# Performance work log

Measured on AMD Instinct MI355X. Metric: run time of the kernel, lower is better.

Reference implementation:

```python
import jax, jax.numpy as jnp
import numpy as np

N_NODES = 50000
N_EDGES = 800000
IN_FEATS = 256
H_FEATS = 256
NUM_CLASSES = 16
NUM_GRAPHS = 64


def _glorot(key, shape):
    lim = float(np.sqrt(6.0 / (shape[0] + shape[1])))
    return jax.random.uniform(key, shape, jnp.float32, -lim, lim)


def setup_inputs() -> dict:
    key = jax.random.key(0)
    ks = jax.random.split(key, 12)
    x = jax.random.normal(ks[0], (N_NODES, IN_FEATS), jnp.float32)
    edge_index = jax.random.randint(ks[1], (2, N_EDGES), 0, N_NODES, jnp.int64)
    batch_vec = jnp.sort(jax.random.randint(ks[2], (N_NODES,), 0, NUM_GRAPHS, jnp.int64))
    W1 = _glorot(ks[3], (IN_FEATS, H_FEATS)); b1 = jnp.zeros((H_FEATS,), jnp.float32)
    W2 = _glorot(ks[4], (H_FEATS, H_FEATS)); b2 = jnp.zeros((H_FEATS,), jnp.float32)
    W3 = _glorot(ks[5], (H_FEATS, H_FEATS)); b3 = jnp.zeros((H_FEATS,), jnp.float32)
    W4 = _glorot(ks[6], (H_FEATS, NUM_CLASSES)); b4 = jnp.zeros((NUM_CLASSES,), jnp.float32)
    return {"x": x, "edge_index": edge_index, "batch_vec": batch_vec,
            "W1": W1, "b1": b1, "W2": W2, "b2": b2,
            "W3": W3, "b3": b3, "W4": W4, "b4": b4}


def gcn_conv(x, W, b, src, dst, deg_inv_sqrt):
    # PyG GCNConv: out = D^{-1/2} (A + I) D^{-1/2} (x W) + b
    h = x @ W  # [N, F_out]
    norm = deg_inv_sqrt[src] * deg_inv_sqrt[dst]  # [E+N]
    msgs = h[src] * norm[:, None]  # gather + scale
    agg = jax.ops.segment_sum(msgs, dst, num_segments=x.shape[0])
    return agg + b


def reference(x, edge_index, batch_vec, W1, b1, W2, b2, W3, b3, W4, b4):
    n = x.shape[0]
    # add self-loops once (shared across layers)
    loops = jnp.arange(n, dtype=edge_index.dtype)
    src = jnp.concatenate([edge_index[0], loops])
    dst = jnp.concatenate([edge_index[1], loops])
    deg = jax.ops.segment_sum(jnp.ones_like(dst, dtype=x.dtype), dst, num_segments=n)
    deg_inv_sqrt = jnp.where(deg > 0, jax.lax.rsqrt(deg), 0.0)

    h = gcn_conv(x, W1, b1, src, dst, deg_inv_sqrt)
    h_copy = jax.nn.relu(h)
    # dropout is identity in eval mode (training=False)
    h = gcn_conv(h_copy, W2, b2, src, dst, deg_inv_sqrt)
    h_copy = jax.nn.relu(jax.nn.relu(h) + h_copy)
    h = gcn_conv(h_copy, W3, b3, src, dst, deg_inv_sqrt)
    h = jax.nn.relu(jax.nn.relu(h) + h_copy)
    h = gcn_conv(h, W4, b4, src, dst, deg_inv_sqrt)

    # global_mean_pool over batch vector
    sums = jax.ops.segment_sum(h, batch_vec, num_segments=NUM_GRAPHS)
    counts = jax.ops.segment_sum(jnp.ones((n,), h.dtype), batch_vec, num_segments=NUM_GRAPHS)
    return sums / jnp.maximum(counts, 1.0)[:, None]
```

## Files before the change

kernel.cpp:

```cpp
#include <hip/hip_runtime.h>
#include <hip/hip_bf16.h>

#define N_NODES 50000
#define N_EDGES 800000
#define F 256
#define NGRAPH 64
#define NCLS 16
#define NBLK_N 196

typedef short short8 __attribute__((ext_vector_type(8)));
typedef float f32x4 __attribute__((ext_vector_type(4)));

__device__ __forceinline__ float bf2f(ushort u) {
    unsigned v = ((unsigned)u) << 16;
    return __uint_as_float(v);
}
__device__ __forceinline__ ushort f2bf(float f) {
    __hip_bfloat16 b = __float2bfloat16(f);
    return *reinterpret_cast<ushort*>(&b);
}


__global__ __launch_bounds__(256) void k_zero_int(int* __restrict__ p, int n) {
    int i = blockIdx.x * 256 + threadIdx.x;
    if (i < n) p[i] = 0;
}

__global__ __launch_bounds__(256) void k_count(const int* __restrict__ dst,
                                               int* __restrict__ ecnt) {
    int e = blockIdx.x * 256 + threadIdx.x;
    if (e < N_EDGES) atomicAdd(&ecnt[dst[e]], 1);
}

__global__ __launch_bounds__(256) void k_dinv(const int* __restrict__ ecnt,
                                              float* __restrict__ dinv) {
    int n = blockIdx.x * 256 + threadIdx.x;
    if (n < N_NODES) dinv[n] = rsqrtf((float)(ecnt[n] + 1));
}

__global__ __launch_bounds__(256) void k_scan_block(const int* __restrict__ ecnt,
                                                    int* __restrict__ rowptr,
                                                    int* __restrict__ blkSum) {
    __shared__ int sh[256];
    int i = blockIdx.x * 256 + threadIdx.x;
    int v = (i < N_NODES) ? ecnt[i] : 0;
    sh[threadIdx.x] = v;
    __syncthreads();
#pragma unroll
    for (int off = 1; off < 256; off <<= 1) {
        int t = (threadIdx.x >= off) ? sh[threadIdx.x - off] : 0;
        __syncthreads();
        sh[threadIdx.x] += t;
        __syncthreads();
    }
    if (i < N_NODES) rowptr[i] = sh[threadIdx.x] - v;
    if (threadIdx.x == 255) blkSum[blockIdx.x] = sh[255];
}

__global__ __launch_bounds__(256) void k_scan_tops(int* __restrict__ blkSum,
                                                   int* __restrict__ blkOff) {
    __shared__ int sh[256];
    int v = (threadIdx.x < NBLK_N) ? blkSum[threadIdx.x] : 0;
    sh[threadIdx.x] = v;
    __syncthreads();
#pragma unroll
    for (int off = 1; off < 256; off <<= 1) {
        int t = (threadIdx.x >= off) ? sh[threadIdx.x - off] : 0;
        __syncthreads();
        sh[threadIdx.x] += t;
        __syncthreads();
    }
    if (threadIdx.x < NBLK_N) blkOff[threadIdx.x] = sh[threadIdx.x] - v;
}

__global__ __launch_bounds__(256) void k_scan_add(int* __restrict__ rowptr,
                                                  const int* __restrict__ blkOff,
                                                  int* __restrict__ cursor) {
    int i = blockIdx.x * 256 + threadIdx.x;
    if (i < N_NODES) {
        int r = rowptr[i] + blkOff[blockIdx.x];
        rowptr[i] = r;
        cursor[i] = r;
    }
    if (i == 0) rowptr[N_NODES] = N_EDGES;
}

__global__ __launch_bounds__(256) void k_fill_csr(const int* __restrict__ src,
                                                  const int* __restrict__ dst,
                                                  const float* __restrict__ dinv,
                                                  int* __restrict__ cursor,
                                                  int* __restrict__ csr_src,
                                                  float* __restrict__ csr_w) {
    int e = blockIdx.x * 256 + threadIdx.x;
    if (e >= N_EDGES) return;
    int s = src[e];
    int d = dst[e];
    int p = atomicAdd(&cursor[d], 1);
    csr_src[p] = s;
    csr_w[p] = dinv[s] * dinv[d];
}


__global__ __launch_bounds__(256) void k_cast_bf16(const float* __restrict__ in,
                                                   ushort* __restrict__ out,
                                                   int n8) {
    int i = blockIdx.x * 256 + threadIdx.x;
    if (i >= n8) return;
    const float4* ip = (const float4*)(in + (size_t)i * 8);
    float4 a = ip[0], b = ip[1];
    short8 v;
    v[0] = (short)f2bf(a.x); v[1] = (short)f2bf(a.y);
    v[2] = (short)f2bf(a.z); v[3] = (short)f2bf(a.w);
    v[4] = (short)f2bf(b.x); v[5] = (short)f2bf(b.y);
    v[6] = (short)f2bf(b.z); v[7] = (short)f2bf(b.w);
    *(short8*)(out + (size_t)i * 8) = v;
}

__global__ __launch_bounds__(256) void k_wpack(const float* __restrict__ W,
                                               ushort* __restrict__ Wp) {
    int idx = blockIdx.x * 256 + threadIdx.x;
    if (idx >= 16 * 8 * 64) return;
    int lane = idx & 63;
    int ks = (idx >> 6) & 7;
    int ctg = idx >> 9;
    int kbase = ks * 32 + (lane >> 4) * 8;
    int col = ctg * 16 + (lane & 15);
    short8 v;
#pragma unroll
    for (int e = 0; e < 8; ++e)
        v[e] = (short)f2bf(W[(size_t)(kbase + e) * 256 + col]);
    *(short8*)(Wp + (size_t)idx * 8) = v;
}


__global__ __launch_bounds__(256, 2) void k_mfma256(const ushort* __restrict__ Ab,
                                                    const ushort* __restrict__ Wp,
                                                    ushort* __restrict__ C) {
    const int t = threadIdx.x;
    const int wv = t >> 6;
    const int l = t & 63;
    const int m0 = blockIdx.x * 64;
    const int colbase = wv * 64;
    const int lrow = l & 15;
    const int lk = (l >> 4) * 8;

    short8 wf[4][8];
    const short8* wp = (const short8*)Wp;
#pragma unroll
    for (int ct = 0; ct < 4; ++ct)
#pragma unroll
        for (int ks = 0; ks < 8; ++ks)
            wf[ct][ks] = wp[(size_t)(((wv * 4 + ct) * 8 + ks) * 64) + l];

#pragma unroll
    for (int msub = 0; msub < 4; ++msub) {
        int arow = m0 + msub * 16 + lrow;
        if (arow >= N_NODES) arow = N_NODES - 1;
        const ushort* ap = Ab + (size_t)arow * F + lk;
        short8 af[8];
#pragma unroll
        for (int ks = 0; ks < 8; ++ks)
            af[ks] = *(const short8*)(ap + ks * 32);

        f32x4 acc[4];
#pragma unroll
        for (int ct = 0; ct < 4; ++ct) acc[ct] = (f32x4){0.f, 0.f, 0.f, 0.f};
#pragma unroll
        for (int ks = 0; ks < 8; ++ks)
#pragma unroll
            for (int ct = 0; ct < 4; ++ct)
                acc[ct] = __builtin_amdgcn_mfma_f32_16x16x32_bf16(af[ks], wf[ct][ks], acc[ct], 0, 0, 0);

        int orow0 = m0 + msub * 16 + (l >> 4) * 4;
#pragma unroll
        for (int ct = 0; ct < 4; ++ct) {
            int ocol = colbase + ct * 16 + (l & 15);
#pragma unroll
            for (int r = 0; r < 4; ++r) {
                int orow = orow0 + r;
                if (orow < N_NODES)
                    C[(size_t)orow * F + ocol] = f2bf(acc[ct][r]);
            }
        }
    }
}


template <int MODE>
__global__ __launch_bounds__(256) void k_gather256(const ushort* __restrict__ H,
                                                   const float* __restrict__ bias,
                                                   const float* __restrict__ dinv,
                                                   const int* __restrict__ rowptr,
                                                   const int* __restrict__ csr_src,
                                                   const float* __restrict__ csr_w,
                                                   const ushort* __restrict__ hc,
                                                   ushort* __restrict__ OUT) {
    int gid = blockIdx.x * 256 + threadIdx.x;
    int n = gid >> 6;
    int lane = gid & 63;
    if (n >= N_NODES) return;
    int c = lane * 4;

    float di = dinv[n];
    float s = di * di;
    const ushort4 h = *(const ushort4*)(H + (size_t)n * F + c);
    const float4 b = *(const float4*)(bias + c);
    float ax = b.x + bf2f(h.x) * s;
    float ay = b.y + bf2f(h.y) * s;
    float az = b.z + bf2f(h.z) * s;
    float aw = b.w + bf2f(h.w) * s;

    int i = rowptr[n];
    const int end = rowptr[n + 1];
    for (; i + 3 < end; i += 4) {
        int s0 = csr_src[i], s1 = csr_src[i + 1], s2 = csr_src[i + 2], s3 = csr_src[i + 3];
        float w0 = csr_w[i], w1 = csr_w[i + 1], w2 = csr_w[i + 2], w3 = csr_w[i + 3];
        const ushort4 v0 = *(const ushort4*)(H + (size_t)s0 * F + c);
        const ushort4 v1 = *(const ushort4*)(H + (size_t)s1 * F + c);
        const ushort4 v2 = *(const ushort4*)(H + (size_t)s2 * F + c);
        const ushort4 v3 = *(const ushort4*)(H + (size_t)s3 * F + c);
        ax += w0 * bf2f(v0.x) + w1 * bf2f(v1.x) + w2 * bf2f(v2.x) + w3 * bf2f(v3.x);
        ay += w0 * bf2f(v0.y) + w1 * bf2f(v1.y) + w2 * bf2f(v2.y) + w3 * bf2f(v3.y);
        az += w0 * bf2f(v0.z) + w1 * bf2f(v1.z) + w2 * bf2f(v2.z) + w3 * bf2f(v3.z);
        aw += w0 * bf2f(v0.w) + w1 * bf2f(v1.w) + w2 * bf2f(v2.w) + w3 * bf2f(v3.w);
    }
    for (; i < end; ++i) {
        int s0 = csr_src[i];
        float w0 = csr_w[i];
        const ushort4 v0 = *(const ushort4*)(H + (size_t)s0 * F + c);
        ax += w0 * bf2f(v0.x); ay += w0 * bf2f(v0.y);
        az += w0 * bf2f(v0.z); aw += w0 * bf2f(v0.w);
    }

    float ox, oy, oz, ow;
    if (MODE == 1) {
        ox = fmaxf(ax, 0.f); oy = fmaxf(ay, 0.f);
        oz = fmaxf(az, 0.f); ow = fmaxf(aw, 0.f);
    } else {
        const ushort4 hv = *(const ushort4*)(hc + (size_t)n * F + c);
        ox = fmaxf(fmaxf(ax, 0.f) + bf2f(hv.x), 0.f);
        oy = fmaxf(fmaxf(ay, 0.f) + bf2f(hv.y), 0.f);
        oz = fmaxf(fmaxf(az, 0.f) + bf2f(hv.z), 0.f);
        ow = fmaxf(fmaxf(aw, 0.f) + bf2f(hv.w), 0.f);
    }
    ushort4 ov;
    ov.x = f2bf(ox); ov.y = f2bf(oy); ov.z = f2bf(oz); ov.w = f2bf(ow);
    *(ushort4*)(OUT + (size_t)n * F + c) = ov;
}


__global__ __launch_bounds__(256) void k_gemm16(const ushort* __restrict__ A,
                                                const float* __restrict__ W4,
                                                float* __restrict__ C) {
    __shared__ float Ws[256][16];
    const int t = threadIdx.x;
    {
        const float4* wp = (const float4*)(W4 + (size_t)t * 16);
        float4 a = wp[0], b = wp[1], c = wp[2], d = wp[3];
        float4* sp = (float4*)&Ws[t][0];
        sp[0] = a; sp[1] = b; sp[2] = c; sp[3] = d;
    }
    __syncthreads();
    int row = blockIdx.x * 256 + t;
    if (row >= N_NODES) return;
    const short8* ap = (const short8*)(A + (size_t)row * F);
    float acc[16];
#pragma unroll
    for (int c = 0; c < 16; ++c) acc[c] = 0.f;
    for (int k8 = 0; k8 < 32; ++k8) {
        short8 a8 = ap[k8];
#pragma unroll
        for (int j = 0; j < 8; ++j) {
            float av = bf2f((ushort)a8[j]);
            const float4* wr = (const float4*)&Ws[k8 * 8 + j][0];
            float4 w0 = wr[0], w1 = wr[1], w2 = wr[2], w3 = wr[3];
            acc[0]  += av * w0.x; acc[1]  += av * w0.y;
            acc[2]  += av * w0.z; acc[3]  += av * w0.w;
            acc[4]  += av * w1.x; acc[5]  += av * w1.y;
            acc[6]  += av * w1.z; acc[7]  += av * w1.w;
            acc[8]  += av * w2.x; acc[9]  += av * w2.y;
            acc[10] += av * w2.z; acc[11] += av * w2.w;
            acc[12] += av * w3.x; acc[13] += av * w3.y;
            acc[14] += av * w3.z; acc[15] += av * w3.w;
        }
    }
    float4* op = (float4*)(C + (size_t)row * 16);
    op[0] = make_float4(acc[0], acc[1], acc[2], acc[3]);
    op[1] = make_float4(acc[4], acc[5], acc[6], acc[7]);
    op[2] = make_float4(acc[8], acc[9], acc[10], acc[11]);
    op[3] = make_float4(acc[12], acc[13], acc[14], acc[15]);
}

__global__ __launch_bounds__(256) void k_gather16(const float* __restrict__ H16,
                                                  const float* __restrict__ bias,
                                                  const float* __restrict__ dinv,
                                                  const int* __restrict__ rowptr,
                                                  const int* __restrict__ csr_src,
                                                  const float* __restrict__ csr_w,
                                                  float* __restrict__ OUT) {
    int gid = blockIdx.x * 256 + threadIdx.x;
    int n = gid >> 2;
    int q = (gid & 3) * 4;
    if (n >= N_NODES) return;

    float di = dinv[n];
    float s = di * di;
    const float4 h = *(const float4*)(H16 + (size_t)n * 16 + q);
    const float4 b = *(const float4*)(bias + q);
    float ax = b.x + h.x * s, ay = b.y + h.y * s, az = b.z + h.z * s, aw = b.w + h.w * s;

    const int end = rowptr[n + 1];
    for (int i = rowptr[n]; i < end; ++i) {
        int s0 = csr_src[i];
        float w0 = csr_w[i];
        const float4 v = *(const float4*)(H16 + (size_t)s0 * 16 + q);
        ax += w0 * v.x; ay += w0 * v.y; az += w0 * v.z; aw += w0 * v.w;
    }
    *(float4*)(OUT + (size_t)n * 16 + q) = make_float4(ax, ay, az, aw);
}


__global__ __launch_bounds__(256) void k_pool_zero(float* __restrict__ pool,
                                                   float* __restrict__ cnt) {
    int i = blockIdx.x * 256 + threadIdx.x;
    if (i < NGRAPH * NCLS) pool[i] = 0.f;
    if (i < NGRAPH) cnt[i] = 0.f;
}

__global__ __launch_bounds__(256) void k_pool(const float* __restrict__ H4,
                                              const int* __restrict__ batch,
                                              float* __restrict__ pool,
                                              float* __restrict__ cnt) {
    __shared__ float ps[NGRAPH][NCLS];
    __shared__ float pc[NGRAPH];
    for (int i = threadIdx.x; i < NGRAPH * NCLS; i += 256) ((float*)ps)[i] = 0.f;
    if (threadIdx.x < NGRAPH) pc[threadIdx.x] = 0.f;
    __syncthreads();
    int n = blockIdx.x * 256 + threadIdx.x;
    if (n < N_NODES) {
        int g = batch[n];
        const float4* hp = (const float4*)(H4 + (size_t)n * 16);
        float4 a = hp[0], b = hp[1], c = hp[2], d = hp[3];
        atomicAdd(&ps[g][0],  a.x); atomicAdd(&ps[g][1],  a.y);
        atomicAdd(&ps[g][2],  a.z); atomicAdd(&ps[g][3],  a.w);
        atomicAdd(&ps[g][4],  b.x); atomicAdd(&ps[g][5],  b.y);
        atomicAdd(&ps[g][6],  b.z); atomicAdd(&ps[g][7],  b.w);
        atomicAdd(&ps[g][8],  c.x); atomicAdd(&ps[g][9],  c.y);
        atomicAdd(&ps[g][10], c.z); atomicAdd(&ps[g][11], c.w);
        atomicAdd(&ps[g][12], d.x); atomicAdd(&ps[g][13], d.y);
        atomicAdd(&ps[g][14], d.z); atomicAdd(&ps[g][15], d.w);
        atomicAdd(&pc[g], 1.f);
    }
    __syncthreads();
    for (int i = threadIdx.x; i < NGRAPH * NCLS; i += 256)
        unsafeAtomicAdd(&pool[i], ((float*)ps)[i]);
    if (threadIdx.x < NGRAPH) unsafeAtomicAdd(&cnt[threadIdx.x], pc[threadIdx.x]);
}

__global__ __launch_bounds__(256) void k_final(const float* __restrict__ pool,
                                               const float* __restrict__ cnt,
                                               float* __restrict__ out) {
    int i = blockIdx.x * 256 + threadIdx.x;
    if (i < NGRAPH * NCLS) out[i] = pool[i] / fmaxf(cnt[i >> 4], 1.f);
}


extern "C" void kernel_launch(void* const* d_in, const int* in_sizes, int n_in,
                              void* d_out, int out_size, void* d_ws, size_t ws_size,
                              hipStream_t stream) {
    const float* x   = (const float*)d_in[0];
    const int*   ei  = (const int*)d_in[1];
    const int*   bvec= (const int*)d_in[2];
    const float* W1  = (const float*)d_in[3];
    const float* b1  = (const float*)d_in[4];
    const float* W2  = (const float*)d_in[5];
    const float* b2  = (const float*)d_in[6];
    const float* W3  = (const float*)d_in[7];
    const float* b3  = (const float*)d_in[8];
    const float* W4  = (const float*)d_in[9];
    const float* b4  = (const float*)d_in[10];
    float* out = (float*)d_out;

    const int* src = ei;
    const int* dst = ei + N_EDGES;

    const size_t NF = (size_t)N_NODES * F;
    float* ws = (float*)d_ws;
    ushort* XA = (ushort*)ws;
    ushort* XB = XA + NF;
    ushort* Hg = XB + NF;
    float*  G16 = (float*)(Hg + NF);
    float*  H4  = G16 + (size_t)N_NODES * 16;
    float* aux  = H4 + (size_t)N_NODES * 16;
    int*   ecnt   = (int*)aux;
    float* dinv   = aux + N_NODES;
    int*   rowptr = (int*)(aux + 2 * N_NODES);
    int*   cursor = (int*)(aux + 3 * N_NODES + 64);
    int*   blkSum = (int*)(aux + 4 * N_NODES + 64);
    int*   blkOff = blkSum + 256;
    int*   csr_src= blkOff + 256;
    float* csr_w  = (float*)(csr_src + N_EDGES);
    float* pool   = csr_w + N_EDGES;
    float* cnt    = pool + NGRAPH * NCLS;
    ushort* Wp1   = (ushort*)(cnt + NGRAPH);
    ushort* Wp2   = Wp1 + 65536;
    ushort* Wp3   = Wp2 + 65536;

    const int BN = NBLK_N;
    const int BE = (N_EDGES + 255) / 256;
    const int BG = (N_NODES * 64 + 255) / 256;
    const int BM = (N_NODES + 63) / 64;
    const int BC = (int)((NF / 8 + 255) / 256);

    k_cast_bf16<<<BC, 256, 0, stream>>>(x, XA, (int)(NF / 8));
    k_wpack<<<32, 256, 0, stream>>>(W1, Wp1);
    k_wpack<<<32, 256, 0, stream>>>(W2, Wp2);
    k_wpack<<<32, 256, 0, stream>>>(W3, Wp3);

    k_zero_int<<<BN, 256, 0, stream>>>(ecnt, N_NODES);
    k_count<<<BE, 256, 0, stream>>>(dst, ecnt);
    k_dinv<<<BN, 256, 0, stream>>>(ecnt, dinv);
    k_scan_block<<<BN, 256, 0, stream>>>(ecnt, rowptr, blkSum);
    k_scan_tops<<<1, 256, 0, stream>>>(blkSum, blkOff);
    k_scan_add<<<BN, 256, 0, stream>>>(rowptr, blkOff, cursor);
    k_fill_csr<<<BE, 256, 0, stream>>>(src, dst, dinv, cursor, csr_src, csr_w);

    k_mfma256<<<BM, 256, 0, stream>>>(XA, Wp1, Hg);
    k_gather256<1><<<BG, 256, 0, stream>>>(Hg, b1, dinv, rowptr, csr_src, csr_w, nullptr, XB);

    k_mfma256<<<BM, 256, 0, stream>>>(XB, Wp2, Hg);
    k_gather256<2><<<BG, 256, 0, stream>>>(Hg, b2, dinv, rowptr, csr_src, csr_w, XB, XA);

    k_mfma256<<<BM, 256, 0, stream>>>(XA, Wp3, Hg);
    k_gather256<2><<<BG, 256, 0, stream>>>(Hg, b3, dinv, rowptr, csr_src, csr_w, XA, XB);

    k_gemm16<<<BN, 256, 0, stream>>>(XB, W4, G16);
    k_gather16<<<(N_NODES * 4 + 255) / 256, 256, 0, stream>>>(G16, b4, dinv, rowptr, csr_src, csr_w, H4);

    k_pool_zero<<<5, 256, 0, stream>>>(pool, cnt);
    k_pool<<<BN, 256, 0, stream>>>(H4, bvec, pool, cnt);
    k_final<<<4, 256, 0, stream>>>(pool, cnt, out);
}
```

Before: 422.8 us.

## Fold degree normalization into GEMM epilogue and use feature-chunked 16-bit CSR gather

The D^{-1/2} source scaling moves into the GEMM epilogue, so the edge aggregation becomes a plain sum followed by one destination scale. This removes the per-edge weight array. Column indices are stored as 16-bit values, which is valid only because the node count is below 65536. The 256-wide gather becomes a kernel where each block handles one 32-feature chunk for 64 destination nodes, with four edge slots per wave reduced by shuffles, so the gathered H slice stays cache-resident. The trade-off is narrower 4-byte loads per lane, more blocks, and bf16 rounding applied after the scaling.

New measurement: 926.4 us. +119.1%, slower.

```diff
diff --git a/kernel.cpp b/kernel.cpp
--- a/kernel.cpp
+++ b/kernel.cpp
@@ -19,6 +19,8 @@
     __hip_bfloat16 b = __float2bfloat16(f);
     return *reinterpret_cast<ushort*>(&b);
 }
+__device__ __forceinline__ float bflo(uint u) { return __uint_as_float(u << 16); }
+__device__ __forceinline__ float bfhi(uint u) { return __uint_as_float(u & 0xffff0000u); }
 
 
 __global__ __launch_bounds__(256) void k_zero_int(int* __restrict__ p, int n) {
@@ -87,17 +89,14 @@
 
 __global__ __launch_bounds__(256) void k_fill_csr(const int* __restrict__ src,
                                                   const int* __restrict__ dst,
-                                                  const float* __restrict__ dinv,
                                                   int* __restrict__ cursor,
-                                                  int* __restrict__ csr_src,
-                                                  float* __restrict__ csr_w) {
+                                                  ushort* __restrict__ csr16) {
     int e = blockIdx.x * 256 + threadIdx.x;
     if (e >= N_EDGES) return;
     int s = src[e];
     int d = dst[e];
     int p = atomicAdd(&cursor[d], 1);
-    csr_src[p] = s;
-    csr_w[p] = dinv[s] * dinv[d];
+    csr16[p] = (ushort)s;
 }
 
 
@@ -135,6 +134,7 @@
 
 __global__ __launch_bounds__(256, 2) void k_mfma256(const ushort* __restrict__ Ab,
                                                     const ushort* __restrict__ Wp,
+                                                    const float* __restrict__ dinv,
                                                     ushort* __restrict__ C) {
     const int t = threadIdx.x;
     const int wv = t >> 6;
@@ -172,6 +172,10 @@
                 acc[ct] = __builtin_amdgcn_mfma_f32_16x16x32_bf16(af[ks], wf[ct][ks], acc[ct], 0, 0, 0);
 
         int orow0 = m0 + msub * 16 + (l >> 4) * 4;
+        float dv[4];
+#pragma unroll
+        for (int r = 0; r < 4; ++r)
+            dv[r] = (orow0 + r < N_NODES) ? dinv[orow0 + r] : 0.f;
 #pragma unroll
         for (int ct = 0; ct < 4; ++ct) {
             int ocol = colbase + ct * 16 + (l & 15);
@@ -179,7 +183,7 @@
             for (int r = 0; r < 4; ++r) {
                 int orow = orow0 + r;
                 if (orow < N_NODES)
-                    C[(size_t)orow * F + ocol] = f2bf(acc[ct][r]);
+                    C[(size_t)orow * F + ocol] = f2bf(acc[ct][r] * dv[r]);
             }
         }
     }
@@ -187,70 +191,73 @@
 
 
 template <int MODE>
-__global__ __launch_bounds__(256) void k_gather256(const ushort* __restrict__ H,
-                                                   const float* __restrict__ bias,
-                                                   const float* __restrict__ dinv,
-                                                   const int* __restrict__ rowptr,
-                                                   const int* __restrict__ csr_src,
-                                                   const float* __restrict__ csr_w,
-                                                   const ushort* __restrict__ hc,
-                                                   ushort* __restrict__ OUT) {
-    int gid = blockIdx.x * 256 + threadIdx.x;
-    int n = gid >> 6;
-    int lane = gid & 63;
-    if (n >= N_NODES) return;
-    int c = lane * 4;
-
-    float di = dinv[n];
-    float s = di * di;
-    const ushort4 h = *(const ushort4*)(H + (size_t)n * F + c);
-    const float4 b = *(const float4*)(bias + c);
-    float ax = b.x + bf2f(h.x) * s;
-    float ay = b.y + bf2f(h.y) * s;
-    float az = b.z + bf2f(h.z) * s;
-    float aw = b.w + bf2f(h.w) * s;
-
-    int i = rowptr[n];
-    const int end = rowptr[n + 1];
-    for (; i + 3 < end; i += 4) {
-        int s0 = csr_src[i], s1 = csr_src[i + 1], s2 = csr_src[i + 2], s3 = csr_src[i + 3];
-        float w0 = csr_w[i], w1 = csr_w[i + 1], w2 = csr_w[i + 2], w3 = csr_w[i + 3];
-        const ushort4 v0 = *(const ushort4*)(H + (size_t)s0 * F + c);
-        const ushort4 v1 = *(const ushort4*)(H + (size_t)s1 * F + c);
-        const ushort4 v2 = *(const ushort4*)(H + (size_t)s2 * F + c);
-        const ushort4 v3 = *(const ushort4*)(H + (size_t)s3 * F + c);
-        ax += w0 * bf2f(v0.x) + w1 * bf2f(v1.x) + w2 * bf2f(v2.x) + w3 * bf2f(v3.x);
-        ay += w0 * bf2f(v0.y) + w1 * bf2f(v1.y) + w2 * bf2f(v2.y) + w3 * bf2f(v3.y);
-        az += w0 * bf2f(v0.z) + w1 * bf2f(v1.z) + w2 * bf2f(v2.z) + w3 * bf2f(v3.z);
-        aw += w0 * bf2f(v0.w) + w1 * bf2f(v1.w) + w2 * bf2f(v2.w) + w3 * bf2f(v3.w);
-    }
-    for (; i < end; ++i) {
-        int s0 = csr_src[i];
-        float w0 = csr_w[i];
-        const ushort4 v0 = *(const ushort4*)(H + (size_t)s0 * F + c);
-        ax += w0 * bf2f(v0.x); ay += w0 * bf2f(v0.y);
-        az += w0 * bf2f(v0.z); aw += w0 * bf2f(v0.w);
-    }
-
-    float ox, oy, oz, ow;
-    if (MODE == 1) {
-        ox = fmaxf(ax, 0.f); oy = fmaxf(ay, 0.f);
-        oz = fmaxf(az, 0.f); ow = fmaxf(aw, 0.f);
-    } else {
-        const ushort4 hv = *(const ushort4*)(hc + (size_t)n * F + c);
-        ox = fmaxf(fmaxf(ax, 0.f) + bf2f(hv.x), 0.f);
-        oy = fmaxf(fmaxf(ay, 0.f) + bf2f(hv.y), 0.f);
-        oz = fmaxf(fmaxf(az, 0.f) + bf2f(hv.z), 0.f);
-        ow = fmaxf(fmaxf(aw, 0.f) + bf2f(hv.w), 0.f);
-    }
-    ushort4 ov;
-    ov.x = f2bf(ox); ov.y = f2bf(oy); ov.z = f2bf(oz); ov.w = f2bf(ow);
-    *(ushort4*)(OUT + (size_t)n * F + c) = ov;
+__global__ __launch_bounds__(256) void k_gatherC(const ushort* __restrict__ H,
+                                                 const float* __restrict__ bias,
+                                                 const float* __restrict__ dinv,
+                                                 const int* __restrict__ rowptr,
+                                                 const ushort* __restrict__ csr16,
+                                                 const ushort* __restrict__ hc,
+                                                 ushort* __restrict__ OUT) {
+    const int chunk = blockIdx.x & 7;
+    const int dblk = blockIdx.x >> 3;
+    const int wv = threadIdx.x >> 6;
+    const int lane = threadIdx.x & 63;
+    const int slot = lane >> 4;
+    const int fl = lane & 15;
+    const int f2 = chunk * 32 + fl * 2;
+
+    const float2 bi = *(const float2*)(bias + f2);
+
+    for (int rep = 0; rep < 16; ++rep) {
+        const int d = dblk * 64 + rep * 4 + wv;
+        if (d >= N_NODES) break;
+
+        const int beg = rowptr[d];
+        const int end = rowptr[d + 1];
+
+        float ax = 0.f, ay = 0.f;
+        int e = beg + slot;
+        for (; e + 4 < end; e += 8) {
+            int s0 = __builtin_nontemporal_load(csr16 + e);
+            int s1 = __builtin_nontemporal_load(csr16 + e + 4);
+            uint u0 = *(const uint*)(H + (size_t)s0 * F + f2);
+            uint u1 = *(const uint*)(H + (size_t)s1 * F + f2);
+            ax += bflo(u0) + bflo(u1);
+            ay += bfhi(u0) + bfhi(u1);
+        }
+        if (e < end) {
+            int s0 = __builtin_nontemporal_load(csr16 + e);
+            uint u0 = *(const uint*)(H + (size_t)s0 * F + f2);
+            ax += bflo(u0);
+            ay += bfhi(u0);
+        }
+        ax += __shfl_xor(ax, 16); ay += __shfl_xor(ay, 16);
+        ax += __shfl_xor(ax, 32); ay += __shfl_xor(ay, 32);
+
+        uint su = *(const uint*)(H + (size_t)d * F + f2);
+        float di = dinv[d];
+        float sx = bi.x + di * (ax + bflo(su));
+        float sy = bi.y + di * (ay + bfhi(su));
+
+        float ox, oy;
+        if (MODE == 1) {
+            ox = fmaxf(sx, 0.f); oy = fmaxf(sy, 0.f);
+        } else {
+            uint hcu = __builtin_nontemporal_load((const uint*)(hc + (size_t)d * F + f2));
+            ox = fmaxf(fmaxf(sx, 0.f) + bflo(hcu), 0.f);
+            oy = fmaxf(fmaxf(sy, 0.f) + bfhi(hcu), 0.f);
+        }
+        if (lane < 16) {
+            uint ov = (uint)f2bf(ox) | ((uint)f2bf(oy) << 16);
+            __builtin_nontemporal_store(ov, (uint*)(OUT + (size_t)d * F + f2));
+        }
+    }
 }
 
 
 __global__ __launch_bounds__(256) void k_gemm16(const ushort* __restrict__ A,
                                                 const float* __restrict__ W4,
+                                                const float* __restrict__ dinv,
                                                 float* __restrict__ C) {
     __shared__ float Ws[256][16];
     const int t = threadIdx.x;
@@ -284,6 +291,9 @@
             acc[14] += av * w3.z; acc[15] += av * w3.w;
         }
     }
+    float dv = dinv[row];
+#pragma unroll
+    for (int c = 0; c < 16; ++c) acc[c] *= dv;
     float4* op = (float4*)(C + (size_t)row * 16);
     op[0] = make_float4(acc[0], acc[1], acc[2], acc[3]);
     op[1] = make_float4(acc[4], acc[5], acc[6], acc[7]);
@@ -295,28 +305,29 @@
                                                   const float* __restrict__ bias,
                                                   const float* __restrict__ dinv,
                                                   const int* __restrict__ rowptr,
-                                                  const int* __restrict__ csr_src,
-                                                  const float* __restrict__ csr_w,
+                                                  const ushort* __restrict__ csr16,
                                                   float* __restrict__ OUT) {
     int gid = blockIdx.x * 256 + threadIdx.x;
     int n = gid >> 2;
     int q = (gid & 3) * 4;
     if (n >= N_NODES) return;
 
-    float di = dinv[n];
-    float s = di * di;
+    float ax = 0.f, ay = 0.f, az = 0.f, aw = 0.f;
+    const int end = rowptr[n + 1];
+    for (int i = rowptr[n]; i < end; ++i) {
+        int s0 = csr16[i];
+        const float4 v = *(const float4*)(H16 + (size_t)s0 * 16 + q);
+        ax += v.x; ay += v.y; az += v.z; aw += v.w;
+    }
     const float4 h = *(const float4*)(H16 + (size_t)n * 16 + q);
     const float4 b = *(const float4*)(bias + q);
-    float ax = b.x + h.x * s, ay = b.y + h.y * s, az = b.z + h.z * s, aw = b.w + h.w * s;
-
-    const int end = rowptr[n + 1];
-    for (int i = rowptr[n]; i < end; ++i) {
-        int s0 = csr_src[i];
-        float w0 = csr_w[i];
-        const float4 v = *(const float4*)(H16 + (size_t)s0 * 16 + q);
-        ax += w0 * v.x; ay += w0 * v.y; az += w0 * v.z; aw += w0 * v.w;
-    }
-    *(float4*)(OUT + (size_t)n * 16 + q) = make_float4(ax, ay, az, aw);
+    float di = dinv[n];
+    float4 o;
+    o.x = b.x + di * (ax + h.x);
+    o.y = b.y + di * (ay + h.y);
+    o.z = b.z + di * (az + h.z);
+    o.w = b.w + di * (aw + h.w);
+    *(float4*)(OUT + (size_t)n * 16 + q) = o;
 }
 
 
@@ -391,31 +402,25 @@
     ushort* Hg = XB + NF;
     float*  G16 = (float*)(Hg + NF);
     float*  H4  = G16 + (size_t)N_NODES * 16;
-    float* aux  = H4 + (size_t)N_NODES * 16;
-    int*   ecnt   = (int*)aux;
-    float* dinv   = aux + N_NODES;
-    int*   rowptr = (int*)(aux + 2 * N_NODES);
-    int*   cursor = (int*)(aux + 3 * N_NODES + 64);
-    int*   blkSum = (int*)(aux + 4 * N_NODES + 64);
-    int*   blkOff = blkSum + 256;
-    int*   csr_src= blkOff + 256;
-    float* csr_w  = (float*)(csr_src + N_EDGES);
-    float* pool   = csr_w + N_EDGES;
-    float* cnt    = pool + NGRAPH * NCLS;
-    ushort* Wp1   = (ushort*)(cnt + NGRAPH);
-    ushort* Wp2   = Wp1 + 65536;
-    ushort* Wp3   = Wp2 + 65536;
+    float*  aux = H4 + (size_t)N_NODES * 16;
+    int*    ecnt   = (int*)aux;
+    float*  dinv   = aux + N_NODES;
+    int*    rowptr = (int*)(aux + 2 * N_NODES);
+    int*    cursor = (int*)(aux + 3 * N_NODES + 64);
+    int*    blkSum = (int*)(aux + 4 * N_NODES + 64);
+    int*    blkOff = blkSum + 256;
+    ushort* csr16  = (ushort*)(blkOff + 256);
+    float*  pool   = (float*)(csr16 + N_EDGES);
+    float*  cnt    = pool + NGRAPH * NCLS;
+    ushort* Wp1    = (ushort*)(cnt + NGRAPH);
+    ushort* Wp2    = Wp1 + 65536;
+    ushort* Wp3    = Wp2 + 65536;
 
     const int BN = NBLK_N;
     const int BE = (N_EDGES + 255) / 256;
-    const int BG = (N_NODES * 64 + 255) / 256;
     const int BM = (N_NODES + 63) / 64;
+    const int BGC = 8 * ((N_NODES + 63) / 64);
     const int BC = (int)((NF / 8 + 255) / 256);
-
-    k_cast_bf16<<<BC, 256, 0, stream>>>(x, XA, (int)(NF / 8));
-    k_wpack<<<32, 256, 0, stream>>>(W1, Wp1);
-    k_wpack<<<32, 256, 0, stream>>>(W2, Wp2);
-    k_wpack<<<32, 256, 0, stream>>>(W3, Wp3);
 
     k_zero_int<<<BN, 256, 0, stream>>>(ecnt, N_NODES);
     k_count<<<BE, 256, 0, stream>>>(dst, ecnt);
@@ -423,19 +428,24 @@
     k_scan_block<<<BN, 256, 0, stream>>>(ecnt, rowptr, blkSum);
     k_scan_tops<<<1, 256, 0, stream>>>(blkSum, blkOff);
     k_scan_add<<<BN, 256, 0, stream>>>(rowptr, blkOff, cursor);
-    k_fill_csr<<<BE, 256, 0, stream>>>(src, dst, dinv, cursor, csr_src, csr_w);
-
-    k_mfma256<<<BM, 256, 0, stream>>>(XA, Wp1, Hg);
-    k_gather256<1><<<BG, 256, 0, stream>>>(Hg, b1, dinv, rowptr, csr_src, csr_w, nullptr, XB);
-
-    k_mfma256<<<BM, 256, 0, stream>>>(XB, Wp2, Hg);
-    k_gather256<2><<<BG, 256, 0, stream>>>(Hg, b2, dinv, rowptr, csr_src, csr_w, XB, XA);
-
-    k_mfma256<<<BM, 256, 0, stream>>>(XA, Wp3, Hg);
-    k_gather256<2><<<BG, 256, 0, stream>>>(Hg, b3, dinv, rowptr, csr_src, csr_w, XA, XB);
-
-    k_gemm16<<<BN, 256, 0, stream>>>(XB, W4, G16);
-    k_gather16<<<(N_NODES * 4 + 255) / 256, 256, 0, stream>>>(G16, b4, dinv, rowptr, csr_src, csr_w, H4);
+    k_fill_csr<<<BE, 256, 0, stream>>>(src, dst, cursor, csr16);
+
+    k_cast_bf16<<<BC, 256, 0, stream>>>(x, XA, (int)(NF / 8));
+    k_wpack<<<32, 256, 0, stream>>>(W1, Wp1);
+    k_wpack<<<32, 256, 0, stream>>>(W2, Wp2);
+    k_wpack<<<32, 256, 0, stream>>>(W3, Wp3);
+
+    k_mfma256<<<BM, 256, 0, stream>>>(XA, Wp1, dinv, Hg);
+    k_gatherC<1><<<BGC, 256, 0, stream>>>(Hg, b1, dinv, rowptr, csr16, nullptr, XB);
+
+    k_mfma256<<<BM, 256, 0, stream>>>(XB, Wp2, dinv, Hg);
+    k_gatherC<2><<<BGC, 256, 0, stream>>>(Hg, b2, dinv, rowptr, csr16, XB, XA);
+
+    k_mfma256<<<BM, 256, 0, stream>>>(XA, Wp3, dinv, Hg);
+    k_gatherC<2><<<BGC, 256, 0, stream>>>(Hg, b3, dinv, rowptr, csr16, XA, XB);
+
+    k_gemm16<<<BN, 256, 0, stream>>>(XB, W4, dinv, G16);
+    k_gather16<<<(N_NODES * 4 + 255) / 256, 256, 0, stream>>>(G16, b4, dinv, rowptr, csr16, H4);
 
     k_pool_zero<<<5, 256, 0, stream>>>(pool, cnt);
     k_pool<<<BN, 256, 0, stream>>>(H4, bvec, pool, cnt);
```
